# Kernel tuning notes

Measured on AMD Instinct MI355X. Metric: run time of the kernel, lower is better.

The kernel has to match this reference:

```python
import jax, jax.numpy as jnp
import numpy as np

PC_RANGE = np.array([-51.2, -51.2, -5.0, 51.2, 51.2, 3.0], dtype=np.float32)
IMG_H, IMG_W = 256.0, 704.0
EPS = 1e-5


def bilinear_sample(feat, grid):
    """torch.grid_sample(bilinear, padding_mode='zeros', align_corners=False).
    feat: [C, H, W]; grid: [M, 2] with (x, y) in [-1, 1]. Returns [C, M]."""
    C, H, W = feat.shape
    x = ((grid[:, 0] + 1.0) * W - 1.0) * 0.5
    y = ((grid[:, 1] + 1.0) * H - 1.0) * 0.5
    x0 = jnp.floor(x); y0 = jnp.floor(y)
    x1 = x0 + 1.0;     y1 = y0 + 1.0
    wx1 = x - x0; wx0 = 1.0 - wx1
    wy1 = y - y0; wy0 = 1.0 - wy1

    def gather(xi, yi, w):
        valid = (xi >= 0) & (xi <= W - 1) & (yi >= 0) & (yi <= H - 1)
        xc = jnp.clip(xi, 0, W - 1).astype(jnp.int32)
        yc = jnp.clip(yi, 0, H - 1).astype(jnp.int32)
        v = feat[:, yc, xc]                      # [C, M]
        return v * (w * valid.astype(w.dtype))[None, :]

    return (gather(x0, y0, wx0 * wy0) + gather(x1, y0, wx1 * wy0)
            + gather(x0, y1, wx0 * wy1) + gather(x1, y1, wx1 * wy1))


def setup_inputs() -> dict:
    key = jax.random.key(0)
    k1, k2, k3, k4 = jax.random.split(key, 4)
    reference_points = jax.random.uniform(k1, (1, 4, 128, 128, 3), dtype=jnp.float32)
    feats0 = jax.random.normal(k2, (1, 6, 128, 32, 88), dtype=jnp.float32)
    feats1 = jax.random.normal(k3, (1, 6, 128, 16, 44), dtype=jnp.float32)
    lidar2img = jax.random.normal(k4, (1, 6, 4, 4), dtype=jnp.float32)
    return {"reference_points": reference_points, "feats0": feats0,
            "feats1": feats1, "lidar2img": lidar2img}


def reference(reference_points, feats0, feats1, lidar2img):
    pc = jnp.asarray(PC_RANGE)
    B, P, Hb, Wb, _ = reference_points.shape
    Q = Hb * Wb
    N = lidar2img.shape[1]
    # 'b p h w d' -> 'b (h w) p d' (T=1 squeezed)
    rp = reference_points.transpose(0, 2, 3, 1, 4).reshape(B, Q, P, 3)
    rp = rp * (pc[3:] - pc[:3]) + pc[:3]                     # denormalize
    pts = jnp.concatenate([rp, jnp.ones_like(rp[..., :1])], axis=-1)  # [B,Q,P,4]
    cam = jnp.einsum('bnij,bqpj->bnqpi', lidar2img, pts)     # [B,N,Q,P,4]
    z = cam[..., 2]
    u = cam[..., 0] / (jnp.maximum(z, EPS) * IMG_W)
    v = cam[..., 1] / (jnp.maximum(z, EPS) * IMG_H)
    mask = (z > EPS) & (u > 0.0) & (u < 1.0) & (v > 0.0) & (v < 1.0)  # [B,N,Q,P]
    grid = jnp.stack([u * 2.0 - 1.0, v * 2.0 - 1.0], axis=-1)  # [B,N,Q,P,2]
    grid_flat = grid.reshape(B * N, Q * P, 2)

    sample = jax.vmap(bilinear_sample)   # over B*N
    acc = None
    for feat in (feats0, feats1):
        C, Hl, Wl = feat.shape[2], feat.shape[3], feat.shape[4]
        s = sample(feat.reshape(B * N, C, Hl, Wl), grid_flat)  # [B*N, C, Q*P]
        acc = s if acc is None else acc + s
    sampled = acc / 2.0                                       # mean over 2 levels
    C = feats0.shape[2]
    sampled = sampled.reshape(B, N, C, Q, P)
    m = mask.astype(sampled.dtype)[:, :, None, :, :]          # [B,N,1,Q,P]
    num = jnp.sum(sampled * m, axis=1)                        # [B,C,Q,P]
    den = jnp.maximum(jnp.sum(m, axis=1), 1.0)
    out = (num / den).transpose(0, 2, 3, 1)                   # [B,Q,P,C]
    return out
```

## Files before the change

### kernel.cpp

```cpp
#include <hip/hip_runtime.h>

#define C_CH 128

__global__ __launch_bounds__(256) void transpose_chw_hwc(
    const float* __restrict__ in, float* __restrict__ out, int C, int HW) {
  __shared__ float tile[32][33];
  int n = blockIdx.z;
  const float* src = in + (size_t)n * C * HW;
  float* dst = out + (size_t)n * C * HW;
  int hw0 = blockIdx.x * 32;
  int c0  = blockIdx.y * 32;
  #pragma unroll
  for (int i = threadIdx.y; i < 32; i += 8) {
    int c  = c0 + i;
    int hw = hw0 + threadIdx.x;
    if (c < C && hw < HW) tile[i][threadIdx.x] = src[(size_t)c * HW + hw];
  }
  __syncthreads();
  #pragma unroll
  for (int i = threadIdx.y; i < 32; i += 8) {
    int hw = hw0 + i;
    int c  = c0 + threadIdx.x;
    if (hw < HW && c < C) dst[(size_t)hw * C + c] = tile[threadIdx.x][i];
  }
}

struct TapW {
  int x0, x1, y0, y1;
  float wx0, wx1, wy0, wy1;
  bool vx0, vx1, vy0, vy1;
};

__device__ __forceinline__ void tap_setup(float u, float v, int H, int W, TapW& t) {
  float gx = u * 2.0f - 1.0f;
  float gy = v * 2.0f - 1.0f;
  float x = ((gx + 1.0f) * (float)W - 1.0f) * 0.5f;
  float y = ((gy + 1.0f) * (float)H - 1.0f) * 0.5f;
  float x0f = floorf(x), y0f = floorf(y);
  t.x0 = (int)x0f; t.y0 = (int)y0f;
  t.x1 = t.x0 + 1; t.y1 = t.y0 + 1;
  t.wx1 = x - x0f; t.wx0 = 1.0f - t.wx1;
  t.wy1 = y - y0f; t.wy0 = 1.0f - t.wy1;
  t.vx0 = (t.x0 >= 0) && (t.x0 < W);
  t.vx1 = (t.x1 >= 0) && (t.x1 < W);
  t.vy0 = (t.y0 >= 0) && (t.y0 < H);
  t.vy1 = (t.y1 >= 0) && (t.y1 < H);
}

__device__ __forceinline__ void samp_hwc(const float* __restrict__ f, int nHW,
                                         int H, int W, float u, float v, int c,
                                         float4& acc) {
  TapW t; tap_setup(u, v, H, W, t);
  const float* b0 = f + (size_t)nHW * C_CH;
  {
    if (t.vx0 && t.vy0) {
      const float4 val = *reinterpret_cast<const float4*>(b0 + ((size_t)t.y0 * W + t.x0) * C_CH + c);
      float wgt = t.wx0 * t.wy0;
      acc.x += val.x * wgt; acc.y += val.y * wgt; acc.z += val.z * wgt; acc.w += val.w * wgt;
    }
    if (t.vx1 && t.vy0) {
      const float4 val = *reinterpret_cast<const float4*>(b0 + ((size_t)t.y0 * W + t.x1) * C_CH + c);
      float wgt = t.wx1 * t.wy0;
      acc.x += val.x * wgt; acc.y += val.y * wgt; acc.z += val.z * wgt; acc.w += val.w * wgt;
    }
    if (t.vx0 && t.vy1) {
      const float4 val = *reinterpret_cast<const float4*>(b0 + ((size_t)t.y1 * W + t.x0) * C_CH + c);
      float wgt = t.wx0 * t.wy1;
      acc.x += val.x * wgt; acc.y += val.y * wgt; acc.z += val.z * wgt; acc.w += val.w * wgt;
    }
    if (t.vx1 && t.vy1) {
      const float4 val = *reinterpret_cast<const float4*>(b0 + ((size_t)t.y1 * W + t.x1) * C_CH + c);
      float wgt = t.wx1 * t.wy1;
      acc.x += val.x * wgt; acc.y += val.y * wgt; acc.z += val.z * wgt; acc.w += val.w * wgt;
    }
  }
}

__device__ __forceinline__ void samp_chw(const float* __restrict__ f, int n,
                                         int H, int W, float u, float v, int c,
                                         float4& acc) {
  TapW t; tap_setup(u, v, H, W, t);
  size_t HW = (size_t)H * W;
  const float* b0 = f + (size_t)n * C_CH * HW + (size_t)c * HW;
  if (t.vx0 && t.vy0) {
    size_t off = (size_t)t.y0 * W + t.x0; float wgt = t.wx0 * t.wy0;
    acc.x += b0[off] * wgt; acc.y += b0[HW + off] * wgt;
    acc.z += b0[2 * HW + off] * wgt; acc.w += b0[3 * HW + off] * wgt;
  }
  if (t.vx1 && t.vy0) {
    size_t off = (size_t)t.y0 * W + t.x1; float wgt = t.wx1 * t.wy0;
    acc.x += b0[off] * wgt; acc.y += b0[HW + off] * wgt;
    acc.z += b0[2 * HW + off] * wgt; acc.w += b0[3 * HW + off] * wgt;
  }
  if (t.vx0 && t.vy1) {
    size_t off = (size_t)t.y1 * W + t.x0; float wgt = t.wx0 * t.wy1;
    acc.x += b0[off] * wgt; acc.y += b0[HW + off] * wgt;
    acc.z += b0[2 * HW + off] * wgt; acc.w += b0[3 * HW + off] * wgt;
  }
  if (t.vx1 && t.vy1) {
    size_t off = (size_t)t.y1 * W + t.x1; float wgt = t.wx1 * t.wy1;
    acc.x += b0[off] * wgt; acc.y += b0[HW + off] * wgt;
    acc.z += b0[2 * HW + off] * wgt; acc.w += b0[3 * HW + off] * wgt;
  }
}

template <bool TRANS>
__global__ __launch_bounds__(256) void bev_kernel(
    const float* __restrict__ rp,
    const float* __restrict__ f0,
    const float* __restrict__ f1,
    const float* __restrict__ l2i,
    float* __restrict__ out)
{
  int lane = threadIdx.x & 31;
  int grp  = threadIdx.x >> 5;
  int pt   = blockIdx.x * 8 + grp;
  int p = pt & 3;
  int q = pt >> 2;
  int h = q >> 7;
  int w = q & 127;
  int c = lane << 2;

  const float* rpp = rp + ((size_t)((p * 128 + h) * 128 + w)) * 3;
  float X = rpp[0] * 102.4f + (-51.2f);
  float Y = rpp[1] * 102.4f + (-51.2f);
  float Z = rpp[2] * 8.0f + (-5.0f);

  float4 acc = make_float4(0.f, 0.f, 0.f, 0.f);
  float cnt = 0.0f;

  for (int n = 0; n < 6; ++n) {
    const float* M = l2i + n * 16;
    float cx = M[0] * X + M[1] * Y + M[2]  * Z + M[3];
    float cy = M[4] * X + M[5] * Y + M[6]  * Z + M[7];
    float cz = M[8] * X + M[9] * Y + M[10] * Z + M[11];
    float dz = fmaxf(cz, 1e-5f);
    float u = cx / (dz * 704.0f);
    float v = cy / (dz * 256.0f);
    bool m = (cz > 1e-5f) && (u > 0.0f) && (u < 1.0f) && (v > 0.0f) && (v < 1.0f);
    if (m) {
      cnt += 1.0f;
      if (TRANS) {
        samp_hwc(f0, n * 32 * 88, 32, 88, u, v, c, acc);
        samp_hwc(f1, n * 16 * 44, 16, 44, u, v, c, acc);
      } else {
        samp_chw(f0, n, 32, 88, u, v, c, acc);
        samp_chw(f1, n, 16, 44, u, v, c, acc);
      }
    }
  }

  float s = 0.5f / fmaxf(cnt, 1.0f);
  float4 o = make_float4(acc.x * s, acc.y * s, acc.z * s, acc.w * s);
  *reinterpret_cast<float4*>(out + (size_t)pt * C_CH + c) = o;
}

extern "C" void kernel_launch(void* const* d_in, const int* in_sizes, int n_in,
                              void* d_out, int out_size, void* d_ws, size_t ws_size,
                              hipStream_t stream) {
  const float* rp  = (const float*)d_in[0];
  const float* f0  = (const float*)d_in[1];
  const float* f1  = (const float*)d_in[2];
  const float* l2i = (const float*)d_in[3];
  float* out = (float*)d_out;

  const size_t n0 = (size_t)6 * 128 * 32 * 88;
  const size_t n1 = (size_t)6 * 128 * 16 * 44;
  const size_t need = (n0 + n1) * sizeof(float);

  if (ws_size >= need) {
    float* f0t = (float*)d_ws;
    float* f1t = f0t + n0;
    dim3 blkT(32, 8, 1);
    transpose_chw_hwc<<<dim3(88, 4, 6), blkT, 0, stream>>>(f0, f0t, 128, 32 * 88);
    transpose_chw_hwc<<<dim3(22, 4, 6), blkT, 0, stream>>>(f1, f1t, 128, 16 * 44);
    bev_kernel<true><<<dim3(8192), dim3(256), 0, stream>>>(rp, f0t, f1t, l2i, out);
  } else {
    bev_kernel<false><<<dim3(8192), dim3(256), 0, stream>>>(rp, f0, f1, l2i, out);
  }
}
```

Baseline: 105.3 us.

## Merge level transposes into one launch and precompute sampling taps in shared memory

The two per-level CHW→HWC transposes become a single launch that picks the level from blockIdx.x. The main kernel now has 48 threads per block compute the projection, mask, bilinear tap offsets and validity-folded weights for each (point, camera) pair and store them in shared memory. Every lane previously repeated that scalar math, so this removes redundant work and makes the gather loop branch-free. The cost is an extra __syncthreads and shared-memory traffic, plus clamped loads even for out-of-bounds taps, which are zero-weighted.

Measured after the change: 89.92 us. 14.6% less time.

```diff
diff --git a/kernel.cpp b/kernel.cpp
--- a/kernel.cpp
+++ b/kernel.cpp
@@ -2,133 +2,149 @@
 
 #define C_CH 128
 
-__global__ __launch_bounds__(256) void transpose_chw_hwc(
-    const float* __restrict__ in, float* __restrict__ out, int C, int HW) {
+__global__ __launch_bounds__(256) void transpose_both(
+    const float* __restrict__ f0, const float* __restrict__ f1,
+    float* __restrict__ o0, float* __restrict__ o1) {
   __shared__ float tile[32][33];
   int n = blockIdx.z;
-  const float* src = in + (size_t)n * C * HW;
-  float* dst = out + (size_t)n * C * HW;
-  int hw0 = blockIdx.x * 32;
+  int lev = (blockIdx.x >= 88) ? 1 : 0;
+  int xt = lev ? (blockIdx.x - 88) : blockIdx.x;
+  int HW = lev ? 704 : 2816;
+  const float* src = (lev ? f1 : f0) + (size_t)n * C_CH * HW;
+  float* dst = (lev ? o1 : o0) + (size_t)n * C_CH * HW;
+  int hw0 = xt * 32;
   int c0  = blockIdx.y * 32;
   #pragma unroll
   for (int i = threadIdx.y; i < 32; i += 8) {
     int c  = c0 + i;
     int hw = hw0 + threadIdx.x;
-    if (c < C && hw < HW) tile[i][threadIdx.x] = src[(size_t)c * HW + hw];
+    if (hw < HW) tile[i][threadIdx.x] = src[(size_t)c * HW + hw];
   }
   __syncthreads();
   #pragma unroll
   for (int i = threadIdx.y; i < 32; i += 8) {
     int hw = hw0 + i;
     int c  = c0 + threadIdx.x;
-    if (hw < HW && c < C) dst[(size_t)hw * C + c] = tile[threadIdx.x][i];
-  }
-}
-
-struct TapW {
-  int x0, x1, y0, y1;
-  float wx0, wx1, wy0, wy1;
-  bool vx0, vx1, vy0, vy1;
-};
-
-__device__ __forceinline__ void tap_setup(float u, float v, int H, int W, TapW& t) {
-  float gx = u * 2.0f - 1.0f;
-  float gy = v * 2.0f - 1.0f;
-  float x = ((gx + 1.0f) * (float)W - 1.0f) * 0.5f;
-  float y = ((gy + 1.0f) * (float)H - 1.0f) * 0.5f;
-  float x0f = floorf(x), y0f = floorf(y);
-  t.x0 = (int)x0f; t.y0 = (int)y0f;
-  t.x1 = t.x0 + 1; t.y1 = t.y0 + 1;
-  t.wx1 = x - x0f; t.wx0 = 1.0f - t.wx1;
-  t.wy1 = y - y0f; t.wy0 = 1.0f - t.wy1;
-  t.vx0 = (t.x0 >= 0) && (t.x0 < W);
-  t.vx1 = (t.x1 >= 0) && (t.x1 < W);
-  t.vy0 = (t.y0 >= 0) && (t.y0 < H);
-  t.vy1 = (t.y1 >= 0) && (t.y1 < H);
-}
-
-__device__ __forceinline__ void samp_hwc(const float* __restrict__ f, int nHW,
-                                         int H, int W, float u, float v, int c,
-                                         float4& acc) {
-  TapW t; tap_setup(u, v, H, W, t);
-  const float* b0 = f + (size_t)nHW * C_CH;
-  {
-    if (t.vx0 && t.vy0) {
-      const float4 val = *reinterpret_cast<const float4*>(b0 + ((size_t)t.y0 * W + t.x0) * C_CH + c);
-      float wgt = t.wx0 * t.wy0;
-      acc.x += val.x * wgt; acc.y += val.y * wgt; acc.z += val.z * wgt; acc.w += val.w * wgt;
-    }
-    if (t.vx1 && t.vy0) {
-      const float4 val = *reinterpret_cast<const float4*>(b0 + ((size_t)t.y0 * W + t.x1) * C_CH + c);
-      float wgt = t.wx1 * t.wy0;
-      acc.x += val.x * wgt; acc.y += val.y * wgt; acc.z += val.z * wgt; acc.w += val.w * wgt;
-    }
-    if (t.vx0 && t.vy1) {
-      const float4 val = *reinterpret_cast<const float4*>(b0 + ((size_t)t.y1 * W + t.x0) * C_CH + c);
-      float wgt = t.wx0 * t.wy1;
-      acc.x += val.x * wgt; acc.y += val.y * wgt; acc.z += val.z * wgt; acc.w += val.w * wgt;
-    }
-    if (t.vx1 && t.vy1) {
-      const float4 val = *reinterpret_cast<const float4*>(b0 + ((size_t)t.y1 * W + t.x1) * C_CH + c);
-      float wgt = t.wx1 * t.wy1;
-      acc.x += val.x * wgt; acc.y += val.y * wgt; acc.z += val.z * wgt; acc.w += val.w * wgt;
-    }
-  }
-}
-
-__device__ __forceinline__ void samp_chw(const float* __restrict__ f, int n,
-                                         int H, int W, float u, float v, int c,
-                                         float4& acc) {
-  TapW t; tap_setup(u, v, H, W, t);
-  size_t HW = (size_t)H * W;
-  const float* b0 = f + (size_t)n * C_CH * HW + (size_t)c * HW;
-  if (t.vx0 && t.vy0) {
-    size_t off = (size_t)t.y0 * W + t.x0; float wgt = t.wx0 * t.wy0;
-    acc.x += b0[off] * wgt; acc.y += b0[HW + off] * wgt;
-    acc.z += b0[2 * HW + off] * wgt; acc.w += b0[3 * HW + off] * wgt;
-  }
-  if (t.vx1 && t.vy0) {
-    size_t off = (size_t)t.y0 * W + t.x1; float wgt = t.wx1 * t.wy0;
-    acc.x += b0[off] * wgt; acc.y += b0[HW + off] * wgt;
-    acc.z += b0[2 * HW + off] * wgt; acc.w += b0[3 * HW + off] * wgt;
-  }
-  if (t.vx0 && t.vy1) {
-    size_t off = (size_t)t.y1 * W + t.x0; float wgt = t.wx0 * t.wy1;
-    acc.x += b0[off] * wgt; acc.y += b0[HW + off] * wgt;
-    acc.z += b0[2 * HW + off] * wgt; acc.w += b0[3 * HW + off] * wgt;
-  }
-  if (t.vx1 && t.vy1) {
-    size_t off = (size_t)t.y1 * W + t.x1; float wgt = t.wx1 * t.wy1;
-    acc.x += b0[off] * wgt; acc.y += b0[HW + off] * wgt;
-    acc.z += b0[2 * HW + off] * wgt; acc.w += b0[3 * HW + off] * wgt;
-  }
-}
-
-template <bool TRANS>
-__global__ __launch_bounds__(256) void bev_kernel(
+    if (hw < HW) dst[(size_t)hw * C_CH + c] = tile[threadIdx.x][i];
+  }
+}
+
+__global__ __launch_bounds__(256) void bev_main(
     const float* __restrict__ rp,
-    const float* __restrict__ f0,
-    const float* __restrict__ f1,
+    const float* __restrict__ f0t,
+    const float* __restrict__ f1t,
     const float* __restrict__ l2i,
     float* __restrict__ out)
 {
+  __shared__ int   s_off[8][6][2][4];
+  __shared__ float s_wt [8][6][2][4];
+  __shared__ float s_flag[8][6];
+
+  int tid = threadIdx.x;
+  int pt0 = blockIdx.x * 8;
+
+  if (tid < 48) {
+    int lp = tid / 6;
+    int n  = tid - lp * 6;
+    int pt = pt0 + lp;
+    int p = pt & 3, q = pt >> 2, h = q >> 7, w = q & 127;
+    const float* rpp = rp + ((size_t)((p * 128 + h) * 128 + w)) * 3;
+    float X = rpp[0] * 102.4f - 51.2f;
+    float Y = rpp[1] * 102.4f - 51.2f;
+    float Z = rpp[2] * 8.0f - 5.0f;
+    const float* M = l2i + n * 16;
+    float cx = fmaf(M[0], X, fmaf(M[1], Y, fmaf(M[2],  Z, M[3])));
+    float cy = fmaf(M[4], X, fmaf(M[5], Y, fmaf(M[6],  Z, M[7])));
+    float cz = fmaf(M[8], X, fmaf(M[9], Y, fmaf(M[10], Z, M[11])));
+    float dz = fmaxf(cz, 1e-5f);
+    float u = cx / (dz * 704.0f);
+    float v = cy / (dz * 256.0f);
+    bool m = (cz > 1e-5f) && (u > 0.0f) && (u < 1.0f) && (v > 0.0f) && (v < 1.0f);
+    s_flag[lp][n] = m ? 1.0f : 0.0f;
+    if (m) {
+      float gx = u * 2.0f - 1.0f;
+      float gy = v * 2.0f - 1.0f;
+      #pragma unroll
+      for (int lev = 0; lev < 2; ++lev) {
+        const int H = lev ? 16 : 32, W = lev ? 44 : 88;
+        const int base = (lev ? n * 16 * 44 : n * 32 * 88) * C_CH;
+        float x = ((gx + 1.0f) * (float)W - 1.0f) * 0.5f;
+        float y = ((gy + 1.0f) * (float)H - 1.0f) * 0.5f;
+        float x0f = floorf(x), y0f = floorf(y);
+        int x0 = (int)x0f, y0 = (int)y0f;
+        int x1 = x0 + 1, y1 = y0 + 1;
+        float wx1 = x - x0f, wx0 = 1.0f - wx1;
+        float wy1 = y - y0f, wy0 = 1.0f - wy1;
+        float vx0 = (x0 >= 0 && x0 < W) ? 1.f : 0.f;
+        float vx1 = (x1 >= 0 && x1 < W) ? 1.f : 0.f;
+        float vy0 = (y0 >= 0 && y0 < H) ? 1.f : 0.f;
+        float vy1 = (y1 >= 0 && y1 < H) ? 1.f : 0.f;
+        int cx0 = min(max(x0, 0), W - 1), cx1 = min(max(x1, 0), W - 1);
+        int cy0 = min(max(y0, 0), H - 1), cy1 = min(max(y1, 0), H - 1);
+        s_off[lp][n][lev][0] = base + (cy0 * W + cx0) * C_CH;
+        s_off[lp][n][lev][1] = base + (cy0 * W + cx1) * C_CH;
+        s_off[lp][n][lev][2] = base + (cy1 * W + cx0) * C_CH;
+        s_off[lp][n][lev][3] = base + (cy1 * W + cx1) * C_CH;
+        s_wt[lp][n][lev][0] = wx0 * wy0 * vx0 * vy0;
+        s_wt[lp][n][lev][1] = wx1 * wy0 * vx1 * vy0;
+        s_wt[lp][n][lev][2] = wx0 * wy1 * vx0 * vy1;
+        s_wt[lp][n][lev][3] = wx1 * wy1 * vx1 * vy1;
+      }
+    }
+  }
+  __syncthreads();
+
+  int lane = tid & 31;
+  int grp  = tid >> 5;
+  int c = lane << 2;
+  float4 acc = make_float4(0.f, 0.f, 0.f, 0.f);
+  float cnt = 0.f;
+  #pragma unroll
+  for (int n = 0; n < 6; ++n) {
+    float flag = s_flag[grp][n];
+    cnt += flag;
+    if (flag != 0.0f) {
+      #pragma unroll
+      for (int t = 0; t < 4; ++t) {
+        float4 val = *reinterpret_cast<const float4*>(f0t + s_off[grp][n][0][t] + c);
+        float wgt = s_wt[grp][n][0][t];
+        acc.x = fmaf(val.x, wgt, acc.x);
+        acc.y = fmaf(val.y, wgt, acc.y);
+        acc.z = fmaf(val.z, wgt, acc.z);
+        acc.w = fmaf(val.w, wgt, acc.w);
+      }
+      #pragma unroll
+      for (int t = 0; t < 4; ++t) {
+        float4 val = *reinterpret_cast<const float4*>(f1t + s_off[grp][n][1][t] + c);
+        float wgt = s_wt[grp][n][1][t];
+        acc.x = fmaf(val.x, wgt, acc.x);
+        acc.y = fmaf(val.y, wgt, acc.y);
+        acc.z = fmaf(val.z, wgt, acc.z);
+        acc.w = fmaf(val.w, wgt, acc.w);
+      }
+    }
+  }
+  float s = 0.5f / fmaxf(cnt, 1.0f);
+  int pt = pt0 + grp;
+  *reinterpret_cast<float4*>(out + (size_t)pt * C_CH + c) =
+      make_float4(acc.x * s, acc.y * s, acc.z * s, acc.w * s);
+}
+
+__global__ __launch_bounds__(256) void bev_fallback(
+    const float* __restrict__ rp, const float* __restrict__ f0,
+    const float* __restrict__ f1, const float* __restrict__ l2i,
+    float* __restrict__ out) {
   int lane = threadIdx.x & 31;
   int grp  = threadIdx.x >> 5;
   int pt   = blockIdx.x * 8 + grp;
-  int p = pt & 3;
-  int q = pt >> 2;
-  int h = q >> 7;
-  int w = q & 127;
+  int p = pt & 3, q = pt >> 2, h = q >> 7, w = q & 127;
   int c = lane << 2;
-
   const float* rpp = rp + ((size_t)((p * 128 + h) * 128 + w)) * 3;
-  float X = rpp[0] * 102.4f + (-51.2f);
-  float Y = rpp[1] * 102.4f + (-51.2f);
-  float Z = rpp[2] * 8.0f + (-5.0f);
-
+  float X = rpp[0] * 102.4f - 51.2f;
+  float Y = rpp[1] * 102.4f - 51.2f;
+  float Z = rpp[2] * 8.0f - 5.0f;
   float4 acc = make_float4(0.f, 0.f, 0.f, 0.f);
   float cnt = 0.0f;
-
   for (int n = 0; n < 6; ++n) {
     const float* M = l2i + n * 16;
     float cx = M[0] * X + M[1] * Y + M[2]  * Z + M[3];
@@ -137,22 +153,36 @@
     float dz = fmaxf(cz, 1e-5f);
     float u = cx / (dz * 704.0f);
     float v = cy / (dz * 256.0f);
-    bool m = (cz > 1e-5f) && (u > 0.0f) && (u < 1.0f) && (v > 0.0f) && (v < 1.0f);
-    if (m) {
-      cnt += 1.0f;
-      if (TRANS) {
-        samp_hwc(f0, n * 32 * 88, 32, 88, u, v, c, acc);
-        samp_hwc(f1, n * 16 * 44, 16, 44, u, v, c, acc);
-      } else {
-        samp_chw(f0, n, 32, 88, u, v, c, acc);
-        samp_chw(f1, n, 16, 44, u, v, c, acc);
+    if (!((cz > 1e-5f) && (u > 0.f) && (u < 1.f) && (v > 0.f) && (v < 1.f))) continue;
+    cnt += 1.0f;
+    float gx = u * 2.0f - 1.0f, gy = v * 2.0f - 1.0f;
+    for (int lev = 0; lev < 2; ++lev) {
+      const int H = lev ? 16 : 32, W = lev ? 44 : 88;
+      const float* f = lev ? f1 : f0;
+      size_t HW = (size_t)H * W;
+      const float* b0 = f + (size_t)n * C_CH * HW + (size_t)c * HW;
+      float x = ((gx + 1.0f) * (float)W - 1.0f) * 0.5f;
+      float y = ((gy + 1.0f) * (float)H - 1.0f) * 0.5f;
+      float x0f = floorf(x), y0f = floorf(y);
+      int x0 = (int)x0f, y0 = (int)y0f, x1 = x0 + 1, y1 = y0 + 1;
+      float wx1 = x - x0f, wx0 = 1.0f - wx1;
+      float wy1 = y - y0f, wy0 = 1.0f - wy1;
+      int xs[4] = {x0, x1, x0, x1}, ys[4] = {y0, y0, y1, y1};
+      float ws4[4] = {wx0 * wy0, wx1 * wy0, wx0 * wy1, wx1 * wy1};
+      for (int t = 0; t < 4; ++t) {
+        if (xs[t] < 0 || xs[t] >= W || ys[t] < 0 || ys[t] >= H) continue;
+        size_t off = (size_t)ys[t] * W + xs[t];
+        float wgt = ws4[t];
+        acc.x = fmaf(b0[off], wgt, acc.x);
+        acc.y = fmaf(b0[HW + off], wgt, acc.y);
+        acc.z = fmaf(b0[2 * HW + off], wgt, acc.z);
+        acc.w = fmaf(b0[3 * HW + off], wgt, acc.w);
       }
     }
   }
-
   float s = 0.5f / fmaxf(cnt, 1.0f);
-  float4 o = make_float4(acc.x * s, acc.y * s, acc.z * s, acc.w * s);
-  *reinterpret_cast<float4*>(out + (size_t)pt * C_CH + c) = o;
+  *reinterpret_cast<float4*>(out + (size_t)pt * C_CH + c) =
+      make_float4(acc.x * s, acc.y * s, acc.z * s, acc.w * s);
 }
 
 extern "C" void kernel_launch(void* const* d_in, const int* in_sizes, int n_in,
@@ -171,11 +201,9 @@
   if (ws_size >= need) {
     float* f0t = (float*)d_ws;
     float* f1t = f0t + n0;
-    dim3 blkT(32, 8, 1);
-    transpose_chw_hwc<<<dim3(88, 4, 6), blkT, 0, stream>>>(f0, f0t, 128, 32 * 88);
-    transpose_chw_hwc<<<dim3(22, 4, 6), blkT, 0, stream>>>(f1, f1t, 128, 16 * 44);
-    bev_kernel<true><<<dim3(8192), dim3(256), 0, stream>>>(rp, f0t, f1t, l2i, out);
+    transpose_both<<<dim3(110, 4, 6), dim3(32, 8, 1), 0, stream>>>(f0, f1, f0t, f1t);
+    bev_main<<<dim3(8192), dim3(256), 0, stream>>>(rp, f0t, f1t, l2i, out);
   } else {
-    bev_kernel<false><<<dim3(8192), dim3(256), 0, stream>>>(rp, f0, f1, l2i, out);
-  }
-}
+    bev_fallback<<<dim3(8192), dim3(256), 0, stream>>>(rp, f0, f1, l2i, out);
+  }
+}
```
